# Kernel optimization log

Hardware: AMD Instinct MI355X
Metric: run time of the kernel (lower is better)

## Reference

```python
import jax, jax.numpy as jnp
import numpy as np

N = 50000       # num_of_nodes
IN = 256        # in_features
HID = 128       # hidden_features
HEADS = 4       # num_of_heads
E = 800000      # num edges
ALPHA = 0.2     # leaky relu slope
EPS = 1e-6      # layernorm eps
SCALE = float(np.sqrt(HID * HEADS))


def setup_inputs() -> dict:
    key = jax.random.key(0)
    ks = jax.random.split(key, 8)
    data = jax.random.normal(ks[0], (N, IN), dtype=jnp.float32)
    edge = jax.random.randint(ks[1], (2, E), 0, N, dtype=jnp.int64)
    embed_table = jax.random.normal(ks[2], (N, IN), dtype=jnp.float32)
    # per-head Linear(in -> hidden): weight [HEADS, HID, IN], bias [HEADS, HID]
    W = jax.random.normal(ks[3], (HEADS, HID, IN), dtype=jnp.float32) / np.sqrt(IN)
    b = jax.random.normal(ks[4], (HEADS, HID), dtype=jnp.float32) * 0.01
    # attention vectors a: torch.rand -> uniform [0,1)
    a_attn = jax.random.uniform(ks[5], (HEADS, 2 * HID), dtype=jnp.float32)
    ln_gain = jnp.ones((HEADS * HID,), dtype=jnp.float32)
    ln_bias = jnp.zeros((HEADS * HID,), dtype=jnp.float32)
    return {"data": data, "edge": edge, "embed_table": embed_table,
            "W": W, "b": b, "a_attn": a_attn,
            "ln_gain": ln_gain, "ln_bias": ln_bias}


def _leaky(x):
    return jnp.where(x >= 0, x, ALPHA * x)


def reference(data, edge, embed_table, W, b, a_attn, ln_gain, ln_bias):
    # concat=True: input `data` is ignored, nodes come from embedding table
    emb = embed_table.at[0].set(0.0)  # padding_idx=0
    src, dst = edge[0], edge[1]
    heads_out = []
    for h in range(HEADS):  # small fixed head loop
        x = emb @ W[h].T + b[h]                      # [N, HID]
        # score_e = a . [x_src ; x_dst] split into per-node projections
        s1 = x @ a_attn[h, :HID]                     # [N]
        s2 = x @ a_attn[h, HID:]                     # [N]
        e = jnp.exp(_leaky(s1[src] + s2[dst]) / SCALE)   # [E]
        rowsum = jax.ops.segment_sum(e, src, num_segments=N)          # [N]
        agg = jax.ops.segment_sum(e[:, None] * x[dst], src, num_segments=N)  # [N, HID]
        denom = jnp.where(rowsum == 0, 1.0, rowsum)[:, None]
        heads_out.append(agg / denom)
    h_prime = jnp.concatenate(heads_out, axis=1)     # [N, HEADS*HID]
    # LayerNorm with torch unbiased std and (std + eps)
    mean = h_prime.mean(-1, keepdims=True)
    std = jnp.std(h_prime, axis=-1, ddof=1, keepdims=True)
    normed = ln_gain * (h_prime - mean) / (std + EPS) + ln_bias
    return jax.nn.elu(normed)
```

## Files before the change

### kernel.cpp

```cpp
#include <hip/hip_runtime.h>
#include <math.h>

#define N_NODES 50000
#define IN_F    256
#define HID     128
#define HEADS   4
#define NE      800000
#define ALPHA   0.2f
#define LN_EPS  1e-6f
#define OUT_F   512
#define INV_SCALE 0.04419417382415922f
#define STRIDE  96

#define GEMM_BLOCKS 782
#define SCAT_BLOCKS 3125
#define FUSED_BLOCKS 3907

typedef __attribute__((ext_vector_type(8))) short bf16x8;
typedef __attribute__((ext_vector_type(4))) float f32x4;

static __device__ __forceinline__ unsigned short f2bf(float f) {
  unsigned int u = __float_as_uint(f);
  unsigned int r = (u + 0x7FFFu + ((u >> 16) & 1u)) >> 16;
  return (unsigned short)r;
}
static __device__ __forceinline__ float bf2f(unsigned short h) {
  return __uint_as_float(((unsigned int)h) << 16);
}

__global__ __launch_bounds__(256) void prep_kernel(const float* __restrict__ W,
    unsigned short* __restrict__ WB, int* __restrict__ count)
{
  int i = blockIdx.x * 256 + threadIdx.x;
  float4 v = ((const float4*)W)[i];
  ushort4 o;
  o.x = f2bf(v.x); o.y = f2bf(v.y); o.z = f2bf(v.z); o.w = f2bf(v.w);
  ((ushort4*)WB)[i] = o;
  if (i < N_NODES / 4) ((int4*)count)[i] = make_int4(0, 0, 0, 0);
}

__global__ __launch_bounds__(256, 2) void gemm_scatter(
    const float* __restrict__ embF, const unsigned short* __restrict__ WB,
    const float* __restrict__ bias, const float* __restrict__ a_attn,
    unsigned short* __restrict__ X, float* __restrict__ sbuf, int M,
    const int* __restrict__ src, const int* __restrict__ dst,
    int* __restrict__ count, unsigned short* __restrict__ rec)
{
  __shared__ unsigned short Wl[32 * 512];
  __shared__ unsigned short Al[4 * 512];
  const int bid = blockIdx.x;
  const int tid = threadIdx.x;

  if (bid % 5 != 0) {
    int sblk = bid - bid / 5 - 1;
    int i = sblk * 256 + tid;
    if (i < NE) {
      int s = min(max(src[i], 0), N_NODES - 1);
      int d = min(max(dst[i], 0), N_NODES - 1);
      int slot = atomicAdd(&count[s], 1);
      if (slot < STRIDE) rec[(size_t)s * STRIDE + slot] = (unsigned short)d;
    }
    return;
  }

  const int w = tid >> 6, lane = tid & 63;
  const int r = lane & 15, q = lane >> 4;
  const int bm = (bid / 5) * 64;
  f32x4 acc[8][4] = {};
  for (int k0 = 0; k0 < IN_F; k0 += 32) {
    __syncthreads();
    #pragma unroll
    for (int i2 = 0; i2 < 8; ++i2) {
      int c = i2 * 256 + tid;
      int rr = c & 15, qq = (c >> 4) & 3, nt = c >> 6;
      const unsigned short* gp = WB + (size_t)(nt * 16 + rr) * IN_F + k0 + qq * 8;
      __builtin_amdgcn_global_load_lds(
          (const __attribute__((address_space(1))) void*)gp,
          (__attribute__((address_space(3))) void*)(Wl + c * 8), 16, 0, 0);
    }
    {
      int c = tid;
      int rr = c & 15, qq = (c >> 4) & 3, mb = c >> 6;
      int row = min(bm + mb * 16 + rr, M - 1);
      const float* ap = embF + (size_t)row * IN_F + k0 + qq * 8;
      float4 f0 = *(const float4*)ap;
      float4 f1 = *(const float4*)(ap + 4);
      if (row == 0) { f0 = make_float4(0.f,0.f,0.f,0.f); f1 = make_float4(0.f,0.f,0.f,0.f); }
      ushort4 u0 = make_ushort4(f2bf(f0.x), f2bf(f0.y), f2bf(f0.z), f2bf(f0.w));
      ushort4 u1 = make_ushort4(f2bf(f1.x), f2bf(f1.y), f2bf(f1.z), f2bf(f1.w));
      *(ushort4*)(Al + c * 8)     = u0;
      *(ushort4*)(Al + c * 8 + 4) = u1;
    }
    __syncthreads();
    bf16x8 bfrag[4];
    #pragma unroll
    for (int mb = 0; mb < 4; ++mb)
      bfrag[mb] = *(const bf16x8*)(Al + mb * 512 + q * 128 + r * 8);
    #pragma unroll
    for (int t = 0; t < 8; ++t) {
      bf16x8 afrag = *(const bf16x8*)(Wl + (w * 8 + t) * 512 + q * 128 + r * 8);
      #pragma unroll
      for (int mb = 0; mb < 4; ++mb)
        acc[t][mb] = __builtin_amdgcn_mfma_f32_16x16x32_bf16(afrag, bfrag[mb], acc[t][mb], 0, 0, 0);
    }
  }
  const float* a1 = a_attn + w * 2 * HID;
  const float* a2 = a1 + HID;
  #pragma unroll
  for (int mb = 0; mb < 4; ++mb) {
    int m = bm + mb * 16 + r;
    float p1 = 0.f, p2 = 0.f;
    #pragma unroll
    for (int t = 0; t < 8; ++t) {
      int nloc = t * 16 + q * 4;
      int n = w * HID + nloc;
      float4 bz = *(const float4*)(bias + n);
      float x0 = acc[t][mb][0] + bz.x;
      float x1 = acc[t][mb][1] + bz.y;
      float x2 = acc[t][mb][2] + bz.z;
      float x3 = acc[t][mb][3] + bz.w;
      float4 av1 = *(const float4*)(a1 + nloc);
      float4 av2 = *(const float4*)(a2 + nloc);
      p1 += x0 * av1.x + x1 * av1.y + x2 * av1.z + x3 * av1.w;
      p2 += x0 * av2.x + x1 * av2.y + x2 * av2.z + x3 * av2.w;
      if (m < M) {
        ushort4 o = make_ushort4(f2bf(x0), f2bf(x1), f2bf(x2), f2bf(x3));
        *(ushort4*)(X + (size_t)m * OUT_F + n) = o;
      }
    }
    p1 += __shfl_xor(p1, 16, 64); p1 += __shfl_xor(p1, 32, 64);
    p2 += __shfl_xor(p2, 16, 64); p2 += __shfl_xor(p2, 32, 64);
    if (q == 0 && m < M) {
      sbuf[(size_t)m * 8 + w]     = p1;
      sbuf[(size_t)m * 8 + 4 + w] = p2;
    }
  }
}

__global__ __launch_bounds__(256) void attn_kernel(const unsigned short* __restrict__ X,
    const unsigned short* __restrict__ rec, const int* __restrict__ count,
    const float* __restrict__ sbuf,
    const float* __restrict__ gain, const float* __restrict__ bias,
    float* __restrict__ out)
{
  const int tid = threadIdx.x;
  const int w = tid >> 6, lane = tid & 63;
  const int n = blockIdx.x * 4 + w;
  if (n >= N_NODES) return;
  const int h = lane >> 4;
  const int c0 = lane * 8;
  const unsigned c0b = (unsigned)(c0 * 2);
  const float s1h = sbuf[(size_t)n * 8 + h];
  const int deg = min(count[n], STRIDE);
  const unsigned short* base = rec + (size_t)n * STRIDE;
  const char* Xb = (const char*)X;
  float acc[8] = {};
  float rowsum = 0.f;
  int i = 0;
  for (; i + 8 <= deg; i += 8) {
    uint4 dw = *(const uint4*)(base + i);
    int d0 = dw.x & 0xFFFF, d1 = dw.x >> 16;
    int d2 = dw.y & 0xFFFF, d3 = dw.y >> 16;
    int d4 = dw.z & 0xFFFF, d5 = dw.z >> 16;
    int d6 = dw.w & 0xFFFF, d7 = dw.w >> 16;
    float t0 = s1h + sbuf[(size_t)d0 * 8 + 4 + h];
    float t1 = s1h + sbuf[(size_t)d1 * 8 + 4 + h];
    float t2 = s1h + sbuf[(size_t)d2 * 8 + 4 + h];
    float t3 = s1h + sbuf[(size_t)d3 * 8 + 4 + h];
    float t4 = s1h + sbuf[(size_t)d4 * 8 + 4 + h];
    float t5 = s1h + sbuf[(size_t)d5 * 8 + 4 + h];
    float t6 = s1h + sbuf[(size_t)d6 * 8 + 4 + h];
    float t7 = s1h + sbuf[(size_t)d7 * 8 + 4 + h];
    bf16x8 x0 = *(const bf16x8*)(Xb + (((unsigned)d0 << 10) + c0b));
    bf16x8 x1 = *(const bf16x8*)(Xb + (((unsigned)d1 << 10) + c0b));
    bf16x8 x2 = *(const bf16x8*)(Xb + (((unsigned)d2 << 10) + c0b));
    bf16x8 x3 = *(const bf16x8*)(Xb + (((unsigned)d3 << 10) + c0b));
    bf16x8 x4 = *(const bf16x8*)(Xb + (((unsigned)d4 << 10) + c0b));
    bf16x8 x5 = *(const bf16x8*)(Xb + (((unsigned)d5 << 10) + c0b));
    bf16x8 x6 = *(const bf16x8*)(Xb + (((unsigned)d6 << 10) + c0b));
    bf16x8 x7 = *(const bf16x8*)(Xb + (((unsigned)d7 << 10) + c0b));
    float e0 = __expf((t0 >= 0.f ? t0 : ALPHA * t0) * INV_SCALE);
    float e1 = __expf((t1 >= 0.f ? t1 : ALPHA * t1) * INV_SCALE);
    float e2 = __expf((t2 >= 0.f ? t2 : ALPHA * t2) * INV_SCALE);
    float e3 = __expf((t3 >= 0.f ? t3 : ALPHA * t3) * INV_SCALE);
    float e4 = __expf((t4 >= 0.f ? t4 : ALPHA * t4) * INV_SCALE);
    float e5 = __expf((t5 >= 0.f ? t5 : ALPHA * t5) * INV_SCALE);
    float e6 = __expf((t6 >= 0.f ? t6 : ALPHA * t6) * INV_SCALE);
    float e7 = __expf((t7 >= 0.f ? t7 : ALPHA * t7) * INV_SCALE);
    rowsum += ((e0 + e1) + (e2 + e3)) + ((e4 + e5) + (e6 + e7));
    #pragma unroll
    for (int j = 0; j < 8; ++j) {
      float s = acc[j];
      s += e0 * bf2f((unsigned short)x0[j]);
      s += e1 * bf2f((unsigned short)x1[j]);
      s += e2 * bf2f((unsigned short)x2[j]);
      s += e3 * bf2f((unsigned short)x3[j]);
      s += e4 * bf2f((unsigned short)x4[j]);
      s += e5 * bf2f((unsigned short)x5[j]);
      s += e6 * bf2f((unsigned short)x6[j]);
      s += e7 * bf2f((unsigned short)x7[j]);
      acc[j] = s;
    }
  }
  for (; i < deg; ++i) {
    int d0 = base[i];
    float t0 = s1h + sbuf[(size_t)d0 * 8 + 4 + h];
    bf16x8 x0 = *(const bf16x8*)(Xb + (((unsigned)d0 << 10) + c0b));
    float e0 = __expf((t0 >= 0.f ? t0 : ALPHA * t0) * INV_SCALE);
    rowsum += e0;
    #pragma unroll
    for (int j = 0; j < 8; ++j)
      acc[j] += e0 * bf2f((unsigned short)x0[j]);
  }
  float inv = (rowsum == 0.f) ? 1.f : 1.f / rowsum;
  float v[8];
  float psum = 0.f, psq = 0.f;
  #pragma unroll
  for (int j = 0; j < 8; ++j) {
    v[j] = acc[j] * inv;
    psum += v[j];
    psq  += v[j] * v[j];
  }
  #pragma unroll
  for (int off = 32; off >= 1; off >>= 1) {
    psum += __shfl_xor(psum, off, 64);
    psq  += __shfl_xor(psq,  off, 64);
  }
  float mean = psum * (1.0f / OUT_F);
  float var  = fmaxf((psq - OUT_F * mean * mean) * (1.0f / (OUT_F - 1)), 0.f);
  float inv_std = 1.0f / (sqrtf(var) + LN_EPS);
  float4 g0 = *(const float4*)(gain + c0);
  float4 g1 = *(const float4*)(gain + c0 + 4);
  float4 bb0 = *(const float4*)(bias + c0);
  float4 bb1 = *(const float4*)(bias + c0 + 4);
  float gg[8] = {g0.x, g0.y, g0.z, g0.w, g1.x, g1.y, g1.z, g1.w};
  float bv[8] = {bb0.x, bb0.y, bb0.z, bb0.w, bb1.x, bb1.y, bb1.z, bb1.w};
  float o[8];
  #pragma unroll
  for (int j = 0; j < 8; ++j) {
    float nv = gg[j] * (v[j] - mean) * inv_std + bv[j];
    o[j] = nv > 0.f ? nv : expm1f(nv);
  }
  float* orow = out + (size_t)n * OUT_F + c0;
  *(float4*)(orow)     = make_float4(o[0], o[1], o[2], o[3]);
  *(float4*)(orow + 4) = make_float4(o[4], o[5], o[6], o[7]);
}

extern "C" void kernel_launch(void* const* d_in, const int* in_sizes, int n_in,
                              void* d_out, int out_size, void* d_ws, size_t ws_size,
                              hipStream_t stream)
{
  const int*   edge   = (const int*)d_in[1];
  const float* embed  = (const float*)d_in[2];
  const float* W      = (const float*)d_in[3];
  const float* b      = (const float*)d_in[4];
  const float* a_attn = (const float*)d_in[5];
  const float* ln_g   = (const float*)d_in[6];
  const float* ln_b   = (const float*)d_in[7];
  float* out = (float*)d_out;

  char* ws = (char*)d_ws;
  size_t off = 0;
  auto alloc = [&](size_t bytes) -> void* {
    void* p = ws + off;
    off = (off + bytes + 255) & ~(size_t)255;
    return p;
  };
  unsigned short* WB   = (unsigned short*)alloc((size_t)OUT_F * IN_F * sizeof(unsigned short));
  unsigned short* X    = (unsigned short*)alloc((size_t)N_NODES * OUT_F * sizeof(unsigned short));
  float* sbuf   = (float*)alloc((size_t)N_NODES * 8 * sizeof(float));
  int*   count  = (int*)alloc((size_t)N_NODES * sizeof(int));
  unsigned short* rec = (unsigned short*)alloc((size_t)N_NODES * STRIDE * sizeof(unsigned short));

  const int* src = edge;
  const int* dst = edge + NE;

  prep_kernel<<<(OUT_F * IN_F / 4) / 256, 256, 0, stream>>>(W, WB, count);

  gemm_scatter<<<FUSED_BLOCKS, 256, 0, stream>>>(embed, WB, b, a_attn, X, sbuf, N_NODES,
                                                 src, dst, count, rec);

  attn_kernel<<<(N_NODES + 3) / 4, 256, 0, stream>>>(X, rec, count, sbuf, ln_g, ln_b, out);
}
```

Baseline: 387.3 us.

## Double-buffer LDS tiles in GEMM to overlap global loads with MFMA

The GEMM part of gemm_scatter now uses two LDS buffers for the W and embedding tiles. The next k-slice is prefetched (async global_load_lds for W, register loads for the embedding) while MFMAs run on the current slice, and one barrier per iteration replaces two. Global load addresses are precomputed once outside the loop. This is meant to hide memory latency in the K loop, at the cost of doubled LDS use (about 36KB per block), which may lower occupancy alongside the co-scheduled scatter blocks.

```diff
diff --git a/kernel.cpp b/kernel.cpp
--- a/kernel.cpp
+++ b/kernel.cpp
@@ -46,8 +46,8 @@
     const int* __restrict__ src, const int* __restrict__ dst,
     int* __restrict__ count, unsigned short* __restrict__ rec)
 {
-  __shared__ unsigned short Wl[32 * 512];
-  __shared__ unsigned short Al[4 * 512];
+  __shared__ unsigned short Wl[2][32 * 512];
+  __shared__ unsigned short Al[2][4 * 512];
   const int bid = blockIdx.x;
   const int tid = threadIdx.x;
 
@@ -66,44 +66,75 @@
   const int w = tid >> 6, lane = tid & 63;
   const int r = lane & 15, q = lane >> 4;
   const int bm = (bid / 5) * 64;
+
+  const unsigned short* wg[8];
+  #pragma unroll
+  for (int i2 = 0; i2 < 8; ++i2) {
+    int c = i2 * 256 + tid;
+    int rr = c & 15, qq = (c >> 4) & 3, nt = c >> 6;
+    wg[i2] = WB + (size_t)(nt * 16 + rr) * IN_F + qq * 8;
+  }
+  const int mbg = tid >> 6, qa = (tid >> 4) & 3, ra = tid & 15;
+  const int arow = min(bm + mbg * 16 + ra, M - 1);
+  const float* ag = embF + (size_t)arow * IN_F + qa * 8;
+  const bool azero = (arow == 0);
+
   f32x4 acc[8][4] = {};
-  for (int k0 = 0; k0 < IN_F; k0 += 32) {
-    __syncthreads();
-    #pragma unroll
-    for (int i2 = 0; i2 < 8; ++i2) {
-      int c = i2 * 256 + tid;
-      int rr = c & 15, qq = (c >> 4) & 3, nt = c >> 6;
-      const unsigned short* gp = WB + (size_t)(nt * 16 + rr) * IN_F + k0 + qq * 8;
-      __builtin_amdgcn_global_load_lds(
-          (const __attribute__((address_space(1))) void*)gp,
-          (__attribute__((address_space(3))) void*)(Wl + c * 8), 16, 0, 0);
-    }
-    {
-      int c = tid;
-      int rr = c & 15, qq = (c >> 4) & 3, mb = c >> 6;
-      int row = min(bm + mb * 16 + rr, M - 1);
-      const float* ap = embF + (size_t)row * IN_F + k0 + qq * 8;
-      float4 f0 = *(const float4*)ap;
-      float4 f1 = *(const float4*)(ap + 4);
-      if (row == 0) { f0 = make_float4(0.f,0.f,0.f,0.f); f1 = make_float4(0.f,0.f,0.f,0.f); }
-      ushort4 u0 = make_ushort4(f2bf(f0.x), f2bf(f0.y), f2bf(f0.z), f2bf(f0.w));
-      ushort4 u1 = make_ushort4(f2bf(f1.x), f2bf(f1.y), f2bf(f1.z), f2bf(f1.w));
-      *(ushort4*)(Al + c * 8)     = u0;
-      *(ushort4*)(Al + c * 8 + 4) = u1;
-    }
-    __syncthreads();
+  float4 f0, f1;
+
+  #pragma unroll
+  for (int i2 = 0; i2 < 8; ++i2) {
+    int c = i2 * 256 + tid;
+    __builtin_amdgcn_global_load_lds(
+        (const __attribute__((address_space(1))) void*)(wg[i2]),
+        (__attribute__((address_space(3))) void*)(&Wl[0][c * 8]), 16, 0, 0);
+  }
+  f0 = *(const float4*)ag;
+  f1 = *(const float4*)(ag + 4);
+  if (azero) { f0 = make_float4(0.f,0.f,0.f,0.f); f1 = make_float4(0.f,0.f,0.f,0.f); }
+  {
+    ushort4 u0 = make_ushort4(f2bf(f0.x), f2bf(f0.y), f2bf(f0.z), f2bf(f0.w));
+    ushort4 u1 = make_ushort4(f2bf(f1.x), f2bf(f1.y), f2bf(f1.z), f2bf(f1.w));
+    *(ushort4*)(&Al[0][tid * 8])     = u0;
+    *(ushort4*)(&Al[0][tid * 8 + 4]) = u1;
+  }
+  __syncthreads();
+
+  for (int ks = 0; ks < 8; ++ks) {
+    const int cur = ks & 1, nxt = cur ^ 1;
+    const int knext = (ks + 1) * 32;
+    if (ks < 7) {
+      #pragma unroll
+      for (int i2 = 0; i2 < 8; ++i2) {
+        int c = i2 * 256 + tid;
+        __builtin_amdgcn_global_load_lds(
+            (const __attribute__((address_space(1))) void*)(wg[i2] + knext),
+            (__attribute__((address_space(3))) void*)(&Wl[nxt][c * 8]), 16, 0, 0);
+      }
+      f0 = *(const float4*)(ag + knext);
+      f1 = *(const float4*)(ag + knext + 4);
+      if (azero) { f0 = make_float4(0.f,0.f,0.f,0.f); f1 = make_float4(0.f,0.f,0.f,0.f); }
+    }
     bf16x8 bfrag[4];
     #pragma unroll
     for (int mb = 0; mb < 4; ++mb)
-      bfrag[mb] = *(const bf16x8*)(Al + mb * 512 + q * 128 + r * 8);
+      bfrag[mb] = *(const bf16x8*)(&Al[cur][mb * 512 + q * 128 + r * 8]);
     #pragma unroll
     for (int t = 0; t < 8; ++t) {
-      bf16x8 afrag = *(const bf16x8*)(Wl + (w * 8 + t) * 512 + q * 128 + r * 8);
+      bf16x8 afrag = *(const bf16x8*)(&Wl[cur][(w * 8 + t) * 512 + q * 128 + r * 8]);
       #pragma unroll
       for (int mb = 0; mb < 4; ++mb)
         acc[t][mb] = __builtin_amdgcn_mfma_f32_16x16x32_bf16(afrag, bfrag[mb], acc[t][mb], 0, 0, 0);
     }
-  }
+    if (ks < 7) {
+      ushort4 u0 = make_ushort4(f2bf(f0.x), f2bf(f0.y), f2bf(f0.z), f2bf(f0.w));
+      ushort4 u1 = make_ushort4(f2bf(f1.x), f2bf(f1.y), f2bf(f1.z), f2bf(f1.w));
+      *(ushort4*)(&Al[nxt][tid * 8])     = u0;
+      *(ushort4*)(&Al[nxt][tid * 8 + 4]) = u1;
+    }
+    __syncthreads();
+  }
+
   const float* a1 = a_attn + w * 2 * HID;
   const float* a2 = a1 + HID;
   #pragma unroll
```

Result: no change. 384.3 us (-0.8%).
